# Optimization experiments

Hardware: AMD Instinct MI355X
Metric: run time of the kernel (lower is better)

Reference implementation:

```python
import jax, jax.numpy as jnp
import numpy as np
import math

EMBED_DIM = 2048
NUM_HEADS = 16
HEAD_DIM = EMBED_DIM // NUM_HEADS
BATCH = 2
SEQ = 2048


def setup_inputs() -> dict:
    key = jax.random.key(0)
    ks = jax.random.split(key, 6)
    scale = 1.0 / math.sqrt(EMBED_DIM)
    x = jax.random.normal(ks[0], (BATCH, SEQ, EMBED_DIM), dtype=jnp.float32)
    mask = jnp.ones((BATCH, SEQ), dtype=jnp.float32)
    Wq = jax.random.normal(ks[1], (EMBED_DIM, EMBED_DIM), dtype=jnp.float32) * scale
    Wk = jax.random.normal(ks[2], (EMBED_DIM, EMBED_DIM), dtype=jnp.float32) * scale
    Wv = jax.random.normal(ks[3], (EMBED_DIM, EMBED_DIM), dtype=jnp.float32) * scale
    Wo = jax.random.normal(ks[4], (EMBED_DIM, EMBED_DIM), dtype=jnp.float32) * scale
    return {"x": x, "mask": mask, "Wq": Wq, "Wk": Wk, "Wv": Wv, "Wo": Wo}


def _rope(q, k, seq_len):
    # q, k: [B, H, S, D]
    d = q.shape[-1]
    position = jnp.arange(seq_len, dtype=jnp.float32)[:, None]          # [S,1]
    freqs = 1.0 / (10000.0 ** (jnp.arange(0, d, 2, dtype=jnp.float32) / d))  # [D/2]
    angles = position * freqs                                            # [S,D/2]
    sin = jnp.concatenate([jnp.sin(angles), jnp.sin(angles)], axis=-1)[None, None]  # [1,1,S,D]
    cos = jnp.concatenate([jnp.cos(angles), jnp.cos(angles)], axis=-1)[None, None]

    def rotate_half(t):
        t1, t2 = jnp.split(t, 2, axis=-1)
        return jnp.concatenate([-t2, t1], axis=-1)

    q = q * cos + rotate_half(q) * sin
    k = k * cos + rotate_half(k) * sin
    return q, k


def reference(x, mask, Wq, Wk, Wv, Wo):
    B, S, E = x.shape
    H, D = NUM_HEADS, HEAD_DIM
    # nn.Linear(y) = y @ W.T
    q = (x @ Wq.T).reshape(B, S, H, D).transpose(0, 2, 1, 3)  # [B,H,S,D]
    k = (x @ Wk.T).reshape(B, S, H, D).transpose(0, 2, 1, 3)
    v = (x @ Wv.T).reshape(B, S, H, D).transpose(0, 2, 1, 3)
    q, k = _rope(q, k, S)
    scores = jnp.einsum('bhqd,bhkd->bhqk', q, k) / math.sqrt(D)  # [B,H,S,S]
    # causal mask (strict upper triangle -> -inf)
    causal = jnp.triu(jnp.full((S, S), -jnp.inf, dtype=scores.dtype), k=1)
    scores = scores + causal[None, None]
    # padding mask: [B,S] -> [B,1,1,S] over keys
    scores = scores + (1.0 - mask)[:, None, None, :] * -1e9
    attn = jax.nn.softmax(scores, axis=-1)
    context = jnp.einsum('bhqk,bhkd->bhqd', attn, v)  # [B,H,S,D]
    context = context.transpose(0, 2, 1, 3).reshape(B, S, E)
    return context @ Wo.T
```

## Files before the change

kernel.cpp:

```cpp
#include <hip/hip_runtime.h>
#include <math.h>

typedef unsigned short u16;
typedef __attribute__((ext_vector_type(8))) short bf16x8;
typedef __attribute__((ext_vector_type(8))) unsigned short u16x8;
typedef __attribute__((ext_vector_type(4))) float f32x4;

#define MFMA(a, b, c) __builtin_amdgcn_mfma_f32_16x16x32_bf16((a), (b), (c), 0, 0, 0)

#define GLOAD_LDS16(g, l)                                                     \
  __builtin_amdgcn_global_load_lds(                                           \
      (const __attribute__((address_space(1))) void*)(g),                     \
      (__attribute__((address_space(3))) void*)(l), 16, 0, 0)

#define DRAIN_VMEM() asm volatile("s_waitcnt vmcnt(0)" ::: "memory")
#define FENCE_LDS()                                                            \
  do {                                                                         \
    asm volatile("s_waitcnt lgkmcnt(0)" ::: "memory");                         \
    __builtin_amdgcn_sched_barrier(0);                                         \
  } while (0)

__device__ __forceinline__ float bf2f(u16 u) {
  union { unsigned int i; float f; } x; x.i = ((unsigned int)u) << 16; return x.f;
}
__device__ __forceinline__ u16 f2bf(float f) {
  union { float f; unsigned int i; } x; x.f = f;
  unsigned int r = x.i + 0x7FFFu + ((x.i >> 16) & 1u);
  return (u16)(r >> 16);
}

__global__ __launch_bounds__(256) void probe_all(const u16* p0, const u16* p1,
                                                 const u16* p2, const u16* p3,
                                                 const u16* p4, const u16* p5,
                                                 int* __restrict__ flags) {
  const u16* ps[6] = {p0, p1, p2, p3, p4, p5};
  const u16* p = ps[blockIdx.x];
  __shared__ int cnt;
  if (threadIdx.x == 0) cnt = 0;
  __syncthreads();
  const u16 u = p[threadIdx.x * 2];
  const int e = (u >> 7) & 0xFF;
  atomicAdd(&cnt, (e >= 110 && e <= 135) ? 1 : 0);
  __syncthreads();
  if (threadIdx.x == 0) flags[blockIdx.x] = (cnt > 128) ? 1 : 0;
}

__global__ __launch_bounds__(256) void prep_all(const void* __restrict__ x_in,
                                                const void* __restrict__ wq_in,
                                                const void* __restrict__ wk_in,
                                                const void* __restrict__ wv_in,
                                                const void* __restrict__ wo_in,
                                                const void* __restrict__ mask_in,
                                                u16* __restrict__ xc,
                                                float* __restrict__ mexp,
                                                const int* __restrict__ flags) {
  const int blk = blockIdx.x;
  if (blk < 12288) {
    const int i = blk * 256 + threadIdx.x;
    const void* in; u16* out; int fi, off;
    if (i < (1 << 20)) {
      in = x_in; out = xc; fi = 0; off = i;
    } else {
      const int k = i - (1 << 20);
      const int seg = k >> 19;
      off = k & ((1 << 19) - 1);
      in = (seg == 0) ? wq_in : (seg == 1) ? wk_in : (seg == 2) ? wv_in : wo_in;
      out = xc + ((size_t)1 << 23) + ((size_t)seg << 22);
      fi = 2 + seg;
    }
    if (flags[fi]) {
      ((u16x8*)out)[off] = ((const u16x8*)in)[off];
    } else {
      const float* f = (const float*)in + (size_t)off * 8;
      u16x8 r;
#pragma unroll
      for (int j = 0; j < 8; ++j) r[j] = f2bf(f[j]);
      ((u16x8*)out)[off] = r;
    }
  } else {
    const int i = (blk - 12288) * 256 + threadIdx.x;
    const float m = flags[1] ? bf2f(((const u16*)mask_in)[i]) : ((const float*)mask_in)[i];
    mexp[i] = (1.0f - m) * -1e9f;
  }
}

__global__ __launch_bounds__(256) void gemm_bt(const u16* __restrict__ A,
                                               const u16* __restrict__ B,
                                               void* __restrict__ dst,
                                               int K, int mode) {
  __shared__ __align__(16) u16 As[2][128 * 64];
  __shared__ __align__(16) u16 Bs[2][128 * 64];
  const int tid  = threadIdx.x;
  const int wave = tid >> 6, lane = tid & 63;
  const int quad = lane >> 4, m16 = lane & 15;
  const int wm = (wave >> 1) * 64, wn = (wave & 1) * 64;
  const size_t bi = (size_t)blockIdx.y * 128;
  const size_t bj = (size_t)blockIdx.x * 128;

  f32x4 acc[4][4];
  const f32x4 fz = {0.f, 0.f, 0.f, 0.f};
#pragma unroll
  for (int i = 0; i < 4; ++i)
#pragma unroll
    for (int j = 0; j < 4; ++j) acc[i][j] = fz;

  const u16* gA[4]; const u16* gB[4]; int lofs[4];
#pragma unroll
  for (int j = 0; j < 4; ++j) {
    const int t  = (wave * 4 + j) * 64 + lane;
    const int r  = t >> 3;
    const int cs = t & 7;
    const int c  = cs ^ (r & 7);
    gA[j] = A + (bi + r) * (size_t)K + c * 8;
    gB[j] = B + (bj + r) * (size_t)K + c * 8;
    lofs[j] = t * 8;
  }

#pragma unroll
  for (int j = 0; j < 4; ++j) GLOAD_LDS16(gA[j], &As[0][lofs[j]]);
#pragma unroll
  for (int j = 0; j < 4; ++j) GLOAD_LDS16(gB[j], &Bs[0][lofs[j]]);

  const int nIter = K >> 6;
  for (int it = 0; it < nIter; ++it) {
    DRAIN_VMEM();
    __syncthreads();
    if (it + 1 < nIter) {
      const int ko = (it + 1) << 6;
      const int nb = (it + 1) & 1;
#pragma unroll
      for (int j = 0; j < 4; ++j) GLOAD_LDS16(gA[j] + ko, &As[nb][lofs[j]]);
#pragma unroll
      for (int j = 0; j < 4; ++j) GLOAD_LDS16(gB[j] + ko, &Bs[nb][lofs[j]]);
    }
    const int cb = it & 1;

    bf16x8 af[2][4], bfv[2][4];
#pragma unroll
    for (int kk = 0; kk < 2; ++kk) {
#pragma unroll
      for (int mt = 0; mt < 4; ++mt) {
        const int m = wm + mt * 16 + m16;
        af[kk][mt] = *(const bf16x8*)&As[cb][m * 64 + ((kk * 4 + quad) ^ (m & 7)) * 8];
      }
#pragma unroll
      for (int nt = 0; nt < 4; ++nt) {
        const int n = wn + nt * 16 + m16;
        bfv[kk][nt] = *(const bf16x8*)&Bs[cb][n * 64 + ((kk * 4 + quad) ^ (n & 7)) * 8];
      }
    }
#pragma unroll
    for (int kk = 0; kk < 2; ++kk)
#pragma unroll
      for (int mt = 0; mt < 4; ++mt)
#pragma unroll
        for (int nt = 0; nt < 4; ++nt)
          acc[mt][nt] = MFMA(af[kk][mt], bfv[kk][nt], acc[mt][nt]);
  }

#pragma unroll
  for (int mt = 0; mt < 4; ++mt) {
#pragma unroll
    for (int nt = 0; nt < 4; ++nt) {
#pragma unroll
      for (int rg = 0; rg < 4; ++rg) {
        const int row = (int)bi + wm + mt * 16 + quad * 4 + rg;
        const int col = (int)bj + wn + nt * 16 + m16;
        const float v = acc[mt][nt][rg];
        if (mode == 2) {
          ((float*)dst)[(size_t)row * 2048 + col] = v;
        } else {
          const int band = col >> 11, lc = col & 2047;
          const int bb = row >> 11, s = row & 2047, hh = lc >> 7, dd = lc & 127;
          const size_t bandbase = (size_t)band * 8388608u;
          const size_t idx = (band == 2)
              ? bandbase + ((((size_t)bb * 16 + hh) * 128 + dd) * 2048 + s)
              : bandbase + ((((size_t)bb * 16 + hh) * 2048 + s) * 128 + dd);
          ((u16*)dst)[idx] = f2bf(v);
        }
      }
    }
  }
}

__global__ __launch_bounds__(256) void rope_kernel(u16* __restrict__ Qr,
                                                   u16* __restrict__ Kr) {
  const int tid = blockIdx.x * 256 + threadIdx.x;
  const int j  = tid & 63;
  const int s  = (tid >> 6) & 2047;
  const int bh = tid >> 17;
  const size_t base = ((size_t)bh * 2048 + s) * 128;
  const float freq = __expf(-(float)j * (9.2103403719761836f / 64.0f));
  float sn, cs;
  sincosf((float)s * freq, &sn, &cs);
  const float qs = 0.08838834764831845f;
  const float q1 = bf2f(Qr[base + j]), q2 = bf2f(Qr[base + j + 64]);
  Qr[base + j]      = f2bf((q1 * cs - q2 * sn) * qs);
  Qr[base + j + 64] = f2bf((q2 * cs + q1 * sn) * qs);
  const float k1 = bf2f(Kr[base + j]), k2 = bf2f(Kr[base + j + 64]);
  Kr[base + j]      = f2bf(k1 * cs - k2 * sn);
  Kr[base + j + 64] = f2bf(k2 * cs + k1 * sn);
}

__global__ __launch_bounds__(256, 2) void flash_attn(const u16* __restrict__ Q,
                                                     const u16* __restrict__ Kg,
                                                     const u16* __restrict__ Vg,
                                                     const float* __restrict__ mexp_g,
                                                     u16* __restrict__ ctx) {
  const int S = 2048, D = 128;
  __shared__ __align__(16) u16 Kt[2][64 * 128];
  __shared__ __align__(16) u16 Vt[128 * 64];
  __shared__ __align__(16) u16 Pt[64 * 64];
  const int tid  = threadIdx.x;
  const int wave = tid >> 6, lane = tid & 63;
  const int quad = lane >> 4, m16 = lane & 15;
  const int px = blockIdx.x >> 1;
  const int hl = blockIdx.x & 1;
  const int bh = blockIdx.y;
  const int b = bh >> 4, h = bh & 15;
  const size_t baseQK = (size_t)bh * S * D;
  const size_t baseV  = (size_t)bh * D * S;

  const u16* gK[4]; const u16* gV[4]; int lK[4], lV[4];
#pragma unroll
  for (int j = 0; j < 4; ++j) {
    const int t = (wave * 4 + j) * 64 + lane;
    {
      const int r = t >> 4, cs = t & 15;
      const int c = (cs & 8) | ((cs ^ r) & 7);
      gK[j] = Kg + baseQK + (size_t)r * D + c * 8;
      lK[j] = t * 8;
    }
    {
      const int d = t >> 3, cs = t & 7;
      const int c = cs ^ (d & 7);
      gV[j] = Vg + baseV + (size_t)d * S + c * 8;
      lV[j] = t * 8;
    }
  }

  const f32x4 fz = {0.f, 0.f, 0.f, 0.f};

  for (int pass = 0; pass < 2; ++pass) {
    const int qtile = pass ? px : 15 - px;
    const int q0 = qtile * 128 + hl * 64;
    const int ktmax = 2 * qtile + hl;

    __syncthreads();

    bf16x8 qf[4];
#pragma unroll
    for (int kb = 0; kb < 4; ++kb)
      qf[kb] = *(const bf16x8*)&Q[baseQK +
          (size_t)(q0 + wave * 16 + m16) * D + kb * 32 + quad * 8];

    float li[4] = {0.f, 0.f, 0.f, 0.f};
    f32x4 oacc[8];
#pragma unroll
    for (int dt = 0; dt < 8; ++dt) oacc[dt] = fz;

#pragma unroll
    for (int j = 0; j < 4; ++j) GLOAD_LDS16(gK[j], &Kt[0][lK[j]]);

    for (int kt = 0; kt <= ktmax; ++kt) {
      const int k0 = kt * 64;
      const int cb = kt & 1;
      DRAIN_VMEM();
      __syncthreads();

#pragma unroll
      for (int j = 0; j < 4; ++j) GLOAD_LDS16(gV[j] + k0, &Vt[lV[j]]);
      float madd[4];
#pragma unroll
      for (int nt = 0; nt < 4; ++nt)
        madd[nt] = mexp_g[b * S + k0 + nt * 16 + m16];
      if (kt < ktmax) {
#pragma unroll
        for (int j = 0; j < 4; ++j)
          GLOAD_LDS16(gK[j] + (size_t)(k0 + 64) * D, &Kt[cb ^ 1][lK[j]]);
      }

      f32x4 sacc[4];
#pragma unroll
      for (int nt = 0; nt < 4; ++nt) sacc[nt] = fz;
#pragma unroll
      for (int nt = 0; nt < 4; ++nt)
#pragma unroll
        for (int kb = 0; kb < 4; ++kb) {
          const int c = kb * 4 + quad;
          const int cs = (c & 8) | ((c ^ m16) & 7);
          bf16x8 kf = *(const bf16x8*)&Kt[cb][(nt * 16 + m16) * 128 + cs * 8];
          sacc[nt] = MFMA(qf[kb], kf, sacc[nt]);
        }

      if (kt < ktmax) { asm volatile("s_waitcnt vmcnt(4)" ::: "memory"); }
      else           { asm volatile("s_waitcnt vmcnt(0)" ::: "memory"); }
      __builtin_amdgcn_sched_barrier(0);

      const int R0   = q0 + wave * 16;
      const int prow = wave * 16 + quad * 4;
      if (k0 + 63 > R0) {
#pragma unroll
        for (int rg = 0; rg < 4; ++rg) {
          const int row = R0 + quad * 4 + rg;
          const int pr  = prow + rg;
          float ps = 0.f;
#pragma unroll
          for (int nt = 0; nt < 4; ++nt) {
            const int col = k0 + nt * 16 + m16;
            const float p = (col > row) ? 0.f : __expf(sacc[nt][rg] + madd[nt]);
            ps += p;
            const int c = nt * 2 + (m16 >> 3);
            Pt[pr * 64 + ((c ^ pr) & 7) * 8 + (m16 & 7)] = f2bf(p);
          }
          li[rg] += ps;
        }
      } else {
#pragma unroll
        for (int rg = 0; rg < 4; ++rg) {
          const int pr = prow + rg;
          float ps = 0.f;
#pragma unroll
          for (int nt = 0; nt < 4; ++nt) {
            const float p = __expf(sacc[nt][rg] + madd[nt]);
            ps += p;
            const int c = nt * 2 + (m16 >> 3);
            Pt[pr * 64 + ((c ^ pr) & 7) * 8 + (m16 & 7)] = f2bf(p);
          }
          li[rg] += ps;
        }
      }
      FENCE_LDS();

#pragma unroll
      for (int kb = 0; kb < 2; ++kb) {
        const int c = kb * 4 + quad;
        const int cs = (c ^ m16) & 7;
        bf16x8 pf = *(const bf16x8*)&Pt[(wave * 16 + m16) * 64 + cs * 8];
#pragma unroll
        for (int dt = 0; dt < 8; ++dt) {
          bf16x8 vf = *(const bf16x8*)&Vt[(dt * 16 + m16) * 64 + cs * 8];
          oacc[dt] = MFMA(pf, vf, oacc[dt]);
        }
      }
    }

#pragma unroll
    for (int rg = 0; rg < 4; ++rg) {
      float ls = li[rg];
#pragma unroll
      for (int mk = 1; mk < 16; mk <<= 1) ls += __shfl_xor(ls, mk, 64);
      const float inv = 1.0f / ls;
      const int srow = q0 + wave * 16 + quad * 4 + rg;
#pragma unroll
      for (int dt = 0; dt < 8; ++dt) {
        const int e = h * 128 + dt * 16 + m16;
        ctx[((size_t)b * S + srow) * 2048 + e] = f2bf(oacc[dt][rg] * inv);
      }
    }
  }
}

extern "C" void kernel_launch(void* const* d_in, const int* in_sizes, int n_in,
                              void* d_out, int out_size, void* d_ws, size_t ws_size,
                              hipStream_t stream) {
  (void)in_sizes; (void)n_in; (void)out_size; (void)ws_size;
  const int Bz = 2, S = 2048, E = 2048, H = 16;
  const size_t NX = (size_t)Bz * S * E;
  const size_t NW = (size_t)E * E;

  char* ws = (char*)d_ws;
  int*   flags = (int*)ws;
  float* mexp  = (float*)(ws + 256);
  u16* xc  = (u16*)(ws + 256 + 16384);
  u16* Wqc = xc + NX;
  u16* Qr  = Wqc + 4 * NW;
  u16* Kr  = Qr + NX;
  u16* Vt  = Kr + NX;
  u16* ctx = Vt + NX;
  u16* Woc = Wqc + 3 * NW;

  probe_all<<<6, 256, 0, stream>>>((const u16*)d_in[0], (const u16*)d_in[1],
                                   (const u16*)d_in[2], (const u16*)d_in[3],
                                   (const u16*)d_in[4], (const u16*)d_in[5], flags);

  prep_all<<<12304, 256, 0, stream>>>(d_in[0], d_in[2], d_in[3], d_in[4],
                                      d_in[5], d_in[1], xc, mexp, flags);

  gemm_bt<<<dim3(48, 32), 256, 0, stream>>>(xc, Wqc, Qr, E, 3);
  rope_kernel<<<(Bz * H * S * 64) / 256, 256, 0, stream>>>(Qr, Kr);
  flash_attn<<<dim3(16, Bz * H), 256, 0, stream>>>(Qr, Kr, Vt, mexp, ctx);
  gemm_bt<<<dim3(16, 32), 256, 0, stream>>>(ctx, Woc, d_out, E, 2);
}
```

Before: 413.2 us.

## Fuse RoPE into QKV GEMM epilogue and swizzle GEMM block order

Applies rotary embedding and Q scaling inside the QKV projection GEMM epilogue. Half-dimension partners are exchanged through LDS between paired waves, which removes the separate rope kernel and its read/write of Q and K. It also remaps block indices so consecutive tiles group per XCD, for better cache locality. The cost is extra sincos work and LDS barriers in the epilogue.

```diff
diff --git a/kernel.cpp b/kernel.cpp
--- a/kernel.cpp
+++ b/kernel.cpp
@@ -94,8 +94,12 @@
   const int wave = tid >> 6, lane = tid & 63;
   const int quad = lane >> 4, m16 = lane & 15;
   const int wm = (wave >> 1) * 64, wn = (wave & 1) * 64;
-  const size_t bi = (size_t)blockIdx.y * 128;
-  const size_t bj = (size_t)blockIdx.x * 128;
+
+  const int nwg  = gridDim.x * gridDim.y;
+  const int orig = blockIdx.y * gridDim.x + blockIdx.x;
+  const int lid  = (orig & 7) * (nwg >> 3) + (orig >> 3);
+  const size_t bi = (size_t)(lid / gridDim.x) * 128;
+  const size_t bj = (size_t)(lid % gridDim.x) * 128;
 
   f32x4 acc[4][4];
   const f32x4 fz = {0.f, 0.f, 0.f, 0.f};
@@ -158,6 +162,49 @@
           acc[mt][nt] = MFMA(af[kk][mt], bfv[kk][nt], acc[mt][nt]);
   }
 
+  if (mode == 3 && (int)(bj >> 11) != 2) {
+    float* xch = (float*)&As[0][0];
+    const int bandq = (int)(bj >> 11);
+    const float qsc = (bandq == 0) ? 0.08838834764831845f : 1.0f;
+#pragma unroll
+    for (int ch = 0; ch < 2; ++ch) {
+      __syncthreads();
+#pragma unroll
+      for (int mh = 0; mh < 2; ++mh)
+#pragma unroll
+        for (int nt = 0; nt < 4; ++nt)
+#pragma unroll
+          for (int rg = 0; rg < 4; ++rg)
+            xch[tid * 32 + mh * 16 + nt * 4 + rg] = acc[ch * 2 + mh][nt][rg];
+      __syncthreads();
+      const int ptid = tid ^ 64;
+#pragma unroll
+      for (int mh = 0; mh < 2; ++mh) {
+        const int mt = ch * 2 + mh;
+#pragma unroll
+        for (int nt = 0; nt < 4; ++nt) {
+          const int col = (int)bj + wn + nt * 16 + m16;
+          const int lc = col & 2047, hh = lc >> 7, dd = lc & 127;
+          const float fr = __expf(-(float)(dd & 63) * (9.2103403719761836f / 64.0f));
+#pragma unroll
+          for (int rg = 0; rg < 4; ++rg) {
+            const int row = (int)bi + wm + mt * 16 + quad * 4 + rg;
+            const int bb = row >> 11, s = row & 2047;
+            float sn, cs2;
+            sincosf((float)s * fr, &sn, &cs2);
+            const float v  = acc[mt][nt][rg];
+            const float v2 = xch[ptid * 32 + mh * 16 + nt * 4 + rg];
+            const float o = (wn == 0) ? (v * cs2 - v2 * sn) : (v * cs2 + v2 * sn);
+            const size_t idx = (size_t)bandq * 8388608u +
+                ((((size_t)bb * 16 + hh) * 2048 + s) * 128 + dd);
+            ((u16*)dst)[idx] = f2bf(o * qsc);
+          }
+        }
+      }
+    }
+    return;
+  }
+
 #pragma unroll
   for (int mt = 0; mt < 4; ++mt) {
 #pragma unroll
@@ -170,36 +217,15 @@
         if (mode == 2) {
           ((float*)dst)[(size_t)row * 2048 + col] = v;
         } else {
-          const int band = col >> 11, lc = col & 2047;
+          const int lc = col & 2047;
           const int bb = row >> 11, s = row & 2047, hh = lc >> 7, dd = lc & 127;
-          const size_t bandbase = (size_t)band * 8388608u;
-          const size_t idx = (band == 2)
-              ? bandbase + ((((size_t)bb * 16 + hh) * 128 + dd) * 2048 + s)
-              : bandbase + ((((size_t)bb * 16 + hh) * 2048 + s) * 128 + dd);
+          const size_t idx = (size_t)2 * 8388608u +
+              ((((size_t)bb * 16 + hh) * 128 + dd) * 2048 + s);
           ((u16*)dst)[idx] = f2bf(v);
         }
       }
     }
   }
-}
-
-__global__ __launch_bounds__(256) void rope_kernel(u16* __restrict__ Qr,
-                                                   u16* __restrict__ Kr) {
-  const int tid = blockIdx.x * 256 + threadIdx.x;
-  const int j  = tid & 63;
-  const int s  = (tid >> 6) & 2047;
-  const int bh = tid >> 17;
-  const size_t base = ((size_t)bh * 2048 + s) * 128;
-  const float freq = __expf(-(float)j * (9.2103403719761836f / 64.0f));
-  float sn, cs;
-  sincosf((float)s * freq, &sn, &cs);
-  const float qs = 0.08838834764831845f;
-  const float q1 = bf2f(Qr[base + j]), q2 = bf2f(Qr[base + j + 64]);
-  Qr[base + j]      = f2bf((q1 * cs - q2 * sn) * qs);
-  Qr[base + j + 64] = f2bf((q2 * cs + q1 * sn) * qs);
-  const float k1 = bf2f(Kr[base + j]), k2 = bf2f(Kr[base + j + 64]);
-  Kr[base + j]      = f2bf(k1 * cs - k2 * sn);
-  Kr[base + j + 64] = f2bf(k2 * cs + k1 * sn);
 }
 
 __global__ __launch_bounds__(256, 2) void flash_attn(const u16* __restrict__ Q,
@@ -379,6 +405,7 @@
   u16* Vt  = Kr + NX;
   u16* ctx = Vt + NX;
   u16* Woc = Wqc + 3 * NW;
+  (void)Kr; (void)Vt;
 
   probe_all<<<6, 256, 0, stream>>>((const u16*)d_in[0], (const u16*)d_in[1],
                                    (const u16*)d_in[2], (const u16*)d_in[3],
@@ -388,7 +415,6 @@
                                       d_in[5], d_in[1], xc, mexp, flags);
 
   gemm_bt<<<dim3(48, 32), 256, 0, stream>>>(xc, Wqc, Qr, E, 3);
-  rope_kernel<<<(Bz * H * S * 64) / 256, 256, 0, stream>>>(Qr, Kr);
-  flash_attn<<<dim3(16, Bz * H), 256, 0, stream>>>(Qr, Kr, Vt, mexp, ctx);
+  flash_attn<<<dim3(16, Bz * H), 256, 0, stream>>>(Qr, Qr + NX, Qr + 2 * NX, mexp, ctx);
   gemm_bt<<<dim3(16, 32), 256, 0, stream>>>(ctx, Woc, d_out, E, 2);
 }
```

Result: slower. 992.1 us (+140.1%).
